# Kernel optimization log

Measured on AMD Instinct MI355X. Metric: run time of the kernel, lower is better.

The kernel has to match this reference:

```python
import jax, jax.numpy as jnp
import numpy as np
from jax import lax

CHAR_EMB = 30      # char_embedding_dim
N_FILT = 30        # num_cnn_filter (depthwise multiplier)
KSIZE = 3          # char_kernel_size
WORD_EMB = 100     # word_embedding_dim
MAX_WLEN = 40      # max_word_len
N_CHARS = 102      # characters.id + 2
VOCAB = 400002     # GloVe 400k + unk + pad


def setup_inputs() -> dict:
    key = jax.random.key(0)
    k1, k2, k3, k4, k5, k6 = jax.random.split(key, 6)
    B, S = 64, 128
    char_ids = jax.random.randint(k1, (B, S, MAX_WLEN), 0, N_CHARS)
    word_ids = jax.random.randint(k2, (B, S), 0, VOCAB)
    bound = (3.0 / CHAR_EMB) ** 0.5
    char_emb = jax.random.uniform(k3, (N_CHARS, CHAR_EMB), minval=-bound, maxval=bound, dtype=jnp.float32)
    # grouped Conv1d: out=CHAR_EMB*N_FILT=900, in_per_group=1, kernel=3 (OIH layout)
    fan = 1 * KSIZE + N_FILT * KSIZE
    xav = (6.0 / fan) ** 0.5
    conv_w = jax.random.uniform(k4, (CHAR_EMB * N_FILT, 1, KSIZE), minval=-xav, maxval=xav, dtype=jnp.float32)
    conv_b = jnp.zeros((CHAR_EMB * N_FILT,), dtype=jnp.float32)
    glove = jax.random.normal(k5, (VOCAB, WORD_EMB), dtype=jnp.float32)
    return {"char_ids": char_ids, "word_ids": word_ids, "char_emb": char_emb,
            "conv_w": conv_w, "conv_b": conv_b, "glove": glove}


def reference(char_ids, word_ids, char_emb, conv_w, conv_b, glove):
    B, S, W = char_ids.shape
    # char embedding lookup: [B,S,W,E] -> NCH layout [B*S, E, W]
    x = char_emb[char_ids]                       # [B,S,W,30]
    x = jnp.transpose(x, (0, 1, 3, 2)).reshape(B * S, CHAR_EMB, W)
    # depthwise (grouped) conv, groups=30, multiplier=30 -> 900 out channels, length W-K+1
    y = lax.conv_general_dilated(
        x, conv_w, window_strides=(1,), padding="VALID",
        dimension_numbers=("NCH", "OIH", "NCH"),
        feature_group_count=CHAR_EMB)            # [B*S, 900, 38]
    y = y + conv_b[None, :, None]
    pooled = jnp.max(y, axis=2).reshape(B, S, CHAR_EMB * N_FILT)  # max-over-time
    glove_e = glove[word_ids]                    # [B,S,100]
    return jnp.concatenate([pooled, glove_e], axis=2)  # [B,S,1000]
```

## Files before the change

### kernel.cpp

```cpp
#include <hip/hip_runtime.h>
#include <hip/hip_bf16.h>

#define CHAR_EMB 30
#define NFILT    30
#define WLEN     40
#define TOUT     38
#define OUTC     900
#define WORD_EMB 100
#define RP2      42

__device__ __forceinline__ float2 F2FMA(float2 w, float2 a, float2 c) {
    return make_float2(fmaf(w.x, a.x, c.x), fmaf(w.y, a.y, c.y));
}
__device__ __forceinline__ float2 F2MUL(float2 w, float2 a) {
    return make_float2(w.x * a.x, w.y * a.y);
}

__global__ __launch_bounds__(256) void encoder_kernel(
    const int*   __restrict__ char_ids,
    const int*   __restrict__ word_ids,
    const float* __restrict__ char_emb,
    const float* __restrict__ conv_w,
    const float* __restrict__ conv_b,
    const float* __restrict__ glove,
    float*       __restrict__ out,
    int BS)
{
    const int nA   = 2 * blockIdx.x;
    const int nB   = nA + 1;
    const bool hasB = (nB < BS);
    const int tid  = threadIdx.x;

    __shared__ int cid[2 * WLEN];
    __shared__ __align__(16) float2 xs[CHAR_EMB * RP2];

    float* orowA = out + (long)nA * (OUTC + WORD_EMB);
    float* orowB = out + (long)nB * (OUTC + WORD_EMB);

    if (tid < 25) {
        const float4* gp = reinterpret_cast<const float4*>(glove + (long)word_ids[nA] * WORD_EMB);
        reinterpret_cast<float4*>(orowA + OUTC)[tid] = gp[tid];
    } else if (tid < 50 && hasB) {
        const int j = tid - 25;
        const float4* gp = reinterpret_cast<const float4*>(glove + (long)word_ids[nB] * WORD_EMB);
        reinterpret_cast<float4*>(orowB + OUTC)[j] = gp[j];
    }

    if (tid < 2 * WLEN) {
        cid[tid] = (tid < WLEN || hasB) ? char_ids[nA * WLEN + tid] : 0;
    }
    __syncthreads();

    for (int i = tid; i < WLEN * CHAR_EMB; i += 256) {
        const int t = i / CHAR_EMB;
        const int c = i - t * CHAR_EMB;
        const float a = char_emb[cid[t] * CHAR_EMB + c];
        const float b = char_emb[cid[WLEN + t] * CHAR_EMB + c];
        xs[c * RP2 + t] = make_float2(a, b);
    }
    __syncthreads();

    if (tid < 240) {
        const int g = tid >> 3;
        const int j = tid & 7;

        float2 xr[WLEN];
        const float4* rp = reinterpret_cast<const float4*>(&xs[g * RP2]);
        #pragma unroll
        for (int k = 0; k < WLEN / 2; ++k) {
            float4 q = rp[k];
            xr[2 * k + 0] = make_float2(q.x, q.y);
            xr[2 * k + 1] = make_float2(q.z, q.w);
        }

        #pragma unroll
        for (int f = j; f < NFILT; f += 8) {
            const int o = g * NFILT + f;
            const float w0 = conv_w[o * 3 + 0];
            const float w1 = conv_w[o * 3 + 1];
            const float w2 = conv_w[o * 3 + 2];
            const float2 W0 = make_float2(w0, w0);
            const float2 W1 = make_float2(w1, w1);
            const float2 W2 = make_float2(w2, w2);

            float mA = -3.4e38f, mB = -3.4e38f;
            #pragma unroll
            for (int i = 0; i < TOUT / 2; ++i) {
                const int t = 2 * i;
                float2 v0 = F2FMA(W0, xr[t],     F2FMA(W1, xr[t + 1], F2MUL(W2, xr[t + 2])));
                float2 v1 = F2FMA(W0, xr[t + 1], F2FMA(W1, xr[t + 2], F2MUL(W2, xr[t + 3])));
                mA = fmaxf(fmaxf(mA, v0.x), v1.x);
                mB = fmaxf(fmaxf(mB, v0.y), v1.y);
            }
            const float b = conv_b[o];
            orowA[o] = mA + b;
            if (hasB) orowB[o] = mB + b;
        }
    }
}

extern "C" void kernel_launch(void* const* d_in, const int* in_sizes, int n_in,
                              void* d_out, int out_size, void* d_ws, size_t ws_size,
                              hipStream_t stream) {
    const int*   char_ids = (const int*)  d_in[0];
    const int*   word_ids = (const int*)  d_in[1];
    const float* char_emb = (const float*)d_in[2];
    const float* conv_w   = (const float*)d_in[3];
    const float* conv_b   = (const float*)d_in[4];
    const float* glove    = (const float*)d_in[5];
    float*       out      = (float*)      d_out;

    const int BS = in_sizes[1];
    const int nblk = (BS + 1) / 2;

    encoder_kernel<<<nblk, 256, 0, stream>>>(
        char_ids, word_ids, char_emb, conv_w, conv_b, glove, out, BS);
}
```

Baseline: 235.0 us.

## Use packed FMA asm, interleave filters, split row loads, move glove copy to idle lanes

Rewrites the depthwise conv inner loop to use inline v_pk_fma_f32/v_pk_mul_f32 and v_max3_f32. It processes all four filter slots per thread interleaved, so the loaded row values are reused across filters. The row is loaded from shared memory in two halves to cut register pressure, and launch bounds request 4 blocks per SM. The glove copy moves from the start of the kernel to the 16 otherwise idle threads (tid>=240), so it now runs alongside the convolution instead of before the shared-memory staging.

```diff
diff --git a/kernel.cpp b/kernel.cpp
--- a/kernel.cpp
+++ b/kernel.cpp
@@ -1,5 +1,4 @@
 #include <hip/hip_runtime.h>
-#include <hip/hip_bf16.h>
 
 #define CHAR_EMB 30
 #define NFILT    30
@@ -9,14 +8,26 @@
 #define WORD_EMB 100
 #define RP2      42
 
-__device__ __forceinline__ float2 F2FMA(float2 w, float2 a, float2 c) {
-    return make_float2(fmaf(w.x, a.x, c.x), fmaf(w.y, a.y, c.y));
+typedef float f32x2 __attribute__((ext_vector_type(2)));
+typedef float f32x4 __attribute__((ext_vector_type(4)));
+
+__device__ __forceinline__ f32x2 pk_fma(f32x2 a, f32x2 b, f32x2 c) {
+    f32x2 d;
+    asm("v_pk_fma_f32 %0, %1, %2, %3" : "=v"(d) : "v"(a), "v"(b), "v"(c));
+    return d;
 }
-__device__ __forceinline__ float2 F2MUL(float2 w, float2 a) {
-    return make_float2(w.x * a.x, w.y * a.y);
+__device__ __forceinline__ f32x2 pk_mul(f32x2 a, f32x2 b) {
+    f32x2 d;
+    asm("v_pk_mul_f32 %0, %1, %2" : "=v"(d) : "v"(a), "v"(b));
+    return d;
+}
+__device__ __forceinline__ float max3f(float a, float b, float c) {
+    float d;
+    asm("v_max3_f32 %0, %1, %2, %3" : "=v"(d) : "v"(a), "v"(b), "v"(c));
+    return d;
 }
 
-__global__ __launch_bounds__(256) void encoder_kernel(
+__global__ __launch_bounds__(256, 4) void encoder_kernel(
     const int*   __restrict__ char_ids,
     const int*   __restrict__ word_ids,
     const float* __restrict__ char_emb,
@@ -32,19 +43,10 @@
     const int tid  = threadIdx.x;
 
     __shared__ int cid[2 * WLEN];
-    __shared__ __align__(16) float2 xs[CHAR_EMB * RP2];
+    __shared__ __align__(16) f32x2 xs[CHAR_EMB * RP2];
 
     float* orowA = out + (long)nA * (OUTC + WORD_EMB);
     float* orowB = out + (long)nB * (OUTC + WORD_EMB);
-
-    if (tid < 25) {
-        const float4* gp = reinterpret_cast<const float4*>(glove + (long)word_ids[nA] * WORD_EMB);
-        reinterpret_cast<float4*>(orowA + OUTC)[tid] = gp[tid];
-    } else if (tid < 50 && hasB) {
-        const int j = tid - 25;
-        const float4* gp = reinterpret_cast<const float4*>(glove + (long)word_ids[nB] * WORD_EMB);
-        reinterpret_cast<float4*>(orowB + OUTC)[j] = gp[j];
-    }
 
     if (tid < 2 * WLEN) {
         cid[tid] = (tid < WLEN || hasB) ? char_ids[nA * WLEN + tid] : 0;
@@ -56,7 +58,8 @@
         const int c = i - t * CHAR_EMB;
         const float a = char_emb[cid[t] * CHAR_EMB + c];
         const float b = char_emb[cid[WLEN + t] * CHAR_EMB + c];
-        xs[c * RP2 + t] = make_float2(a, b);
+        f32x2 v; v.x = a; v.y = b;
+        xs[c * RP2 + t] = v;
     }
     __syncthreads();
 
@@ -64,37 +67,106 @@
         const int g = tid >> 3;
         const int j = tid & 7;
 
-        float2 xr[WLEN];
-        const float4* rp = reinterpret_cast<const float4*>(&xs[g * RP2]);
+        f32x2 W0[4], W1[4], W2[4];
+        float bias[4];
+        int   oc[4];
         #pragma unroll
-        for (int k = 0; k < WLEN / 2; ++k) {
-            float4 q = rp[k];
-            xr[2 * k + 0] = make_float2(q.x, q.y);
-            xr[2 * k + 1] = make_float2(q.z, q.w);
+        for (int u = 0; u < 4; ++u) {
+            const int f = j + 8 * u;
+            float w0 = 0.f, w1 = 0.f, w2 = 0.f, bb = 0.f;
+            if (f < NFILT) {
+                const int o = g * NFILT + f;
+                oc[u] = o;
+                w0 = conv_w[o * 3 + 0];
+                w1 = conv_w[o * 3 + 1];
+                w2 = conv_w[o * 3 + 2];
+                bb = conv_b[o];
+            } else {
+                oc[u] = -1;
+            }
+            W0[u].x = w0; W0[u].y = w0;
+            W1[u].x = w1; W1[u].y = w1;
+            W2[u].x = w2; W2[u].y = w2;
+            bias[u] = bb;
+        }
+
+        f32x2 m[4];
+        #pragma unroll
+        for (int u = 0; u < 4; ++u) { m[u].x = -3.4e38f; m[u].y = -3.4e38f; }
+
+        const f32x4* rp = reinterpret_cast<const f32x4*>(&xs[g * RP2]);
+
+        {
+            f32x4 q[11];
+            #pragma unroll
+            for (int k = 0; k < 11; ++k) q[k] = rp[k];
+            #define XA(t) (((t) & 1) ? q[(t) >> 1].zw : q[(t) >> 1].xy)
+            #pragma unroll
+            for (int i = 0; i < 10; ++i) {
+                const f32x2 x0 = XA(2 * i + 0);
+                const f32x2 x1 = XA(2 * i + 1);
+                const f32x2 x2 = XA(2 * i + 2);
+                const f32x2 x3 = XA(2 * i + 3);
+                #pragma unroll
+                for (int u = 0; u < 4; ++u) {
+                    const f32x2 v0 = pk_fma(W0[u], x0, pk_fma(W1[u], x1, pk_mul(W2[u], x2)));
+                    const f32x2 v1 = pk_fma(W0[u], x1, pk_fma(W1[u], x2, pk_mul(W2[u], x3)));
+                    m[u].x = max3f(m[u].x, v0.x, v1.x);
+                    m[u].y = max3f(m[u].y, v0.y, v1.y);
+                }
+            }
+            #undef XA
+        }
+
+        {
+            f32x4 q[10];
+            #pragma unroll
+            for (int k = 0; k < 10; ++k) q[k] = rp[10 + k];
+            #define XB(s) (((s) & 1) ? q[(s) >> 1].zw : q[(s) >> 1].xy)
+            #pragma unroll
+            for (int i = 0; i < 9; ++i) {
+                const int s = 2 * i;
+                const f32x2 x0 = XB(s + 0);
+                const f32x2 x1 = XB(s + 1);
+                const f32x2 x2 = XB(s + 2);
+                const f32x2 x3 = XB(s + 3);
+                #pragma unroll
+                for (int u = 0; u < 4; ++u) {
+                    const f32x2 v0 = pk_fma(W0[u], x0, pk_fma(W1[u], x1, pk_mul(W2[u], x2)));
+                    const f32x2 v1 = pk_fma(W0[u], x1, pk_fma(W1[u], x2, pk_mul(W2[u], x3)));
+                    m[u].x = max3f(m[u].x, v0.x, v1.x);
+                    m[u].y = max3f(m[u].y, v0.y, v1.y);
+                }
+            }
+            #undef XB
         }
 
         #pragma unroll
-        for (int f = j; f < NFILT; f += 8) {
-            const int o = g * NFILT + f;
-            const float w0 = conv_w[o * 3 + 0];
-            const float w1 = conv_w[o * 3 + 1];
-            const float w2 = conv_w[o * 3 + 2];
-            const float2 W0 = make_float2(w0, w0);
-            const float2 W1 = make_float2(w1, w1);
-            const float2 W2 = make_float2(w2, w2);
-
-            float mA = -3.4e38f, mB = -3.4e38f;
+        for (int u = 0; u < 4; ++u) {
+            if (oc[u] >= 0) {
+                orowA[oc[u]] = m[u].x + bias[u];
+                if (hasB) orowB[oc[u]] = m[u].y + bias[u];
+            }
+        }
+    } else {
+        const int k = tid - 240;
+        {
+            const f32x4* gp = reinterpret_cast<const f32x4*>(glove + (long)word_ids[nA] * WORD_EMB);
+            f32x4* op = reinterpret_cast<f32x4*>(orowA + OUTC);
             #pragma unroll
-            for (int i = 0; i < TOUT / 2; ++i) {
-                const int t = 2 * i;
-                float2 v0 = F2FMA(W0, xr[t],     F2FMA(W1, xr[t + 1], F2MUL(W2, xr[t + 2])));
-                float2 v1 = F2FMA(W0, xr[t + 1], F2FMA(W1, xr[t + 2], F2MUL(W2, xr[t + 3])));
-                mA = fmaxf(fmaxf(mA, v0.x), v1.x);
-                mB = fmaxf(fmaxf(mB, v0.y), v1.y);
+            for (int q = 0; q < 2; ++q) {
+                const int idx = k + 16 * q;
+                if (idx < WORD_EMB / 4) op[idx] = gp[idx];
             }
-            const float b = conv_b[o];
-            orowA[o] = mA + b;
-            if (hasB) orowB[o] = mB + b;
+        }
+        if (hasB) {
+            const f32x4* gp = reinterpret_cast<const f32x4*>(glove + (long)word_ids[nB] * WORD_EMB);
+            f32x4* op = reinterpret_cast<f32x4*>(orowB + OUTC);
+            #pragma unroll
+            for (int q = 0; q < 2; ++q) {
+                const int idx = k + 16 * q;
+                if (idx < WORD_EMB / 4) op[idx] = gp[idx];
+            }
         }
     }
 }
```

Result: faster. 228.5 us (-2.7%).
